# Kernel tuning notes

Measured on AMD Instinct MI355X. Metric: run time of the kernel, lower is better.

The kernel has to match this reference:

```python
import jax, jax.numpy as jnp
import numpy as np

LANDMARKS = 80
POINT_LANDMARKS = tuple(range(468, 538))  # 70 hand-region indices
AVG_SET = [[0,40],[40,40],[80,60],[140,60],[200,60],[260,60],[320,50],[370,50],[420,60],[480,63]]
STAT_CAP = 168


def nan_mean(x, axis=0):
    m = jnp.isnan(x)
    num = jnp.where(m, 0.0, x).sum(axis)
    den = jnp.where(m, 0.0, 1.0).sum(axis)
    return num / den


def nan_std(x, axis=0):
    d = x - nan_mean(x, axis=axis)
    return jnp.sqrt(nan_mean(d * d, axis=axis))


def flatten_means_and_stds(x, reshape1):
    # x: [t, L, C] -> stats over frames -> [2L, C] -> (1, reshape1*2)
    out = jnp.concatenate([nan_mean(x, 0), nan_std(x, 0)], axis=0)
    if out.shape[0] > STAT_CAP:
        out = out[:STAT_CAP, :]
    out = out.reshape(1, reshape1 * 2)
    return jnp.where(jnp.isfinite(out), out, jnp.zeros_like(out))


def setup_inputs() -> dict:
    key = jax.random.key(0)
    T, N, C = 32768, 543, 3
    x_in = jax.random.normal(key, (T, N, C), dtype=jnp.float32)
    return {
        "x_in": x_in,
        "num_frames": 16384,
        "segments": 4,
        "input_shape": (16384, 240),
    }


def reference(x_in, num_frames, segments, input_shape):
    # 1) cluster means + point gather -> x: [T, LANDMARKS, 3]
    parts = [jnp.mean(x_in[:, s:s + l, :], axis=1, keepdims=True) for s, l in AVG_SET]
    parts.append(x_in[:, jnp.array(POINT_LANDMARKS), :])
    x = jnp.concatenate(parts, axis=1)

    # 2) symmetric padding loop (axis 1), gated on T % segments as in the original
    xp = x
    rem = x.shape[0] % segments  # shapes are static -> Python int
    for i in range(segments):
        p0 = 1 if (rem > 0 and i % 2 != 0) else 0
        p1 = 1 if (rem > 0 and i % 2 == 0) else 0
        if p0 or p1:
            xp = jnp.pad(xp, ((0, 0), (p0, p1), (0, 0)), mode='symmetric')

    # 3) per-segment nan mean/std stats
    segs = np.array_split(np.arange(xp.shape[0]), segments)
    feats = [flatten_means_and_stds(xp[idx[0]:idx[-1] + 1], input_shape[1]) for idx in segs]
    feats.append(flatten_means_and_stds(x, input_shape[1]))

    # 4) bilinear resize (align_corners=False semantics, no antialias)
    xi = jnp.transpose(x, (2, 0, 1))[None]            # [1, 3, T, L]
    xi = jax.image.resize(xi, (1, 3, num_frames, LANDMARKS), method='bilinear', antialias=False)
    xi = jnp.transpose(xi[0], (1, 2, 0))              # [num_frames, L, 3]
    xi = xi.reshape(1, input_shape[0] * input_shape[1])
    xi = jnp.where(jnp.isnan(xi), jnp.zeros_like(xi), xi)
    feats.append(xi)

    return jnp.concatenate(feats, axis=1)
```

## Files before the change

### kernel.cpp

```cpp
#include <hip/hip_runtime.h>
#include <math.h>

#define T_FRAMES   32768
#define N_LM       543
#define FRAME      1629
#define FPB        16
#define NBLOCKS    (T_FRAMES / FPB)
#define TILES      4
#define TILE_F4    1629
#define OUT_B_OFF  2400
#define ACC_FLOATS 1920

__constant__ int   c_astart[10] = {0, 40, 80, 140, 200, 260, 320, 370, 420, 480};
__constant__ int   c_alen[10]   = {40, 40, 60, 60, 60, 60, 50, 50, 60, 63};

__global__ void zero_acc_kernel(float* __restrict__ acc) {
    int i = blockIdx.x * 256 + threadIdx.x;
    if (i < ACC_FLOATS) acc[i] = 0.0f;
}

__global__ __launch_bounds__(256, 6) void featgen_main(
    const float* __restrict__ xin, float* __restrict__ out, float* __restrict__ acc)
{
    __shared__ float rows[4 * FRAME];

    const int t = threadIdx.x;
    const int b = blockIdx.x;
    const float* src = xin + (size_t)b * (FPB * FRAME);

    const int g8 = t >> 3;
    const int j8 = t & 7;
    int a_s = 0, a_n = 0, a_c = 0;
    float a_inv = 0.0f;
    if (g8 < 30) {
        int l = g8 / 3; a_c = g8 - 3 * l;
        a_s = c_astart[l]; a_n = c_alen[l];
        a_inv = 1.0f / (float)a_n;
    }

    float ssum = 0.0f, ssq = 0.0f;
    float lsum = 0.0f, lsq = 0.0f;

    float4 pre[7];

    {
        const float4* s4 = (const float4*)src;
        #pragma unroll
        for (int i = 0; i < 7; ++i) {
            int idx = t + i * 256;
            if (idx < TILE_F4) pre[i] = s4[idx];
        }
        float4* d4 = (float4*)rows;
        #pragma unroll
        for (int i = 0; i < 7; ++i) {
            int idx = t + i * 256;
            if (idx < TILE_F4) d4[idx] = pre[i];
        }
    }
    __syncthreads();

    for (int grp = 0; grp < TILES; ++grp) {
        if (grp < TILES - 1) {
            const float4* s4 = (const float4*)(src + (size_t)(grp + 1) * (4 * FRAME));
            #pragma unroll
            for (int i = 0; i < 7; ++i) {
                int idx = t + i * 256;
                if (idx < TILE_F4) pre[i] = s4[idx];
            }
        }

        const size_t row0 = (size_t)b * (FPB / 2) + (size_t)grp * 2;

        if (g8 < 30) {
            float v[4];
            #pragma unroll
            for (int f = 0; f < 4; ++f) {
                const float* row = rows + f * FRAME;
                float s = 0.0f;
                for (int j = j8; j < a_n; j += 8) s += row[(a_s + j) * 3 + a_c];
                s += __shfl_xor(s, 1, 8);
                s += __shfl_xor(s, 2, 8);
                s += __shfl_xor(s, 4, 8);
                v[f] = s * a_inv;
            }
            if (j8 == 0) {
                out[OUT_B_OFF + row0 * 240 + g8]       = 0.5f * (v[0] + v[1]);
                out[OUT_B_OFF + (row0 + 1) * 240 + g8] = 0.5f * (v[2] + v[3]);
                lsum += v[0] + v[1] + v[2] + v[3];
                lsq  += v[0]*v[0] + v[1]*v[1] + v[2]*v[2] + v[3]*v[3];
            }
        }

        if (t >= 30 && t < 240) {
            float v0 = rows[0 * FRAME + t + 1374];
            float v1 = rows[1 * FRAME + t + 1374];
            float v2 = rows[2 * FRAME + t + 1374];
            float v3 = rows[3 * FRAME + t + 1374];
            out[OUT_B_OFF + row0 * 240 + t]       = 0.5f * (v0 + v1);
            out[OUT_B_OFF + (row0 + 1) * 240 + t] = 0.5f * (v2 + v3);
            ssum += v0 + v1 + v2 + v3;
            ssq  += v0*v0 + v1*v1 + v2*v2 + v3*v3;
        }

        __syncthreads();

        if (grp < TILES - 1) {
            float4* d4 = (float4*)rows;
            #pragma unroll
            for (int i = 0; i < 7; ++i) {
                int idx = t + i * 256;
                if (idx < TILE_F4) d4[idx] = pre[i];
            }
            __syncthreads();
        }
    }

    const int seg = b >> 9;
    if (g8 < 30 && j8 == 0) {
        atomicAdd(&acc[seg * 480 + g8],       lsum);
        atomicAdd(&acc[seg * 480 + 240 + g8], lsq);
    }
    if (t >= 30 && t < 240) {
        atomicAdd(&acc[seg * 480 + t],       ssum);
        atomicAdd(&acc[seg * 480 + 240 + t], ssq);
    }
}

__global__ __launch_bounds__(256) void finalize_stats(
    const float* __restrict__ acc, float* __restrict__ out)
{
    const int f = blockIdx.x;
    const int t = threadIdx.x;
    if (t >= 240) return;
    float s, q, n;
    if (f < 4) {
        s = acc[f * 480 + t];
        q = acc[f * 480 + 240 + t];
        n = 8192.0f;
    } else {
        s = acc[t]       + acc[480 + t]  + acc[960 + t]  + acc[1440 + t];
        q = acc[240 + t] + acc[720 + t]  + acc[1200 + t] + acc[1680 + t];
        n = 32768.0f;
    }
    float mean = s / n;
    float var  = q / n - mean * mean;
    var = var < 0.0f ? 0.0f : var;
    out[f * 480 + t]       = mean;
    out[f * 480 + 240 + t] = sqrtf(var);
}

extern "C" void kernel_launch(void* const* d_in, const int* in_sizes, int n_in,
                              void* d_out, int out_size, void* d_ws, size_t ws_size,
                              hipStream_t stream) {
    (void)in_sizes; (void)n_in; (void)out_size; (void)ws_size;
    const float* xin = (const float*)d_in[0];
    float* out = (float*)d_out;
    float* acc = (float*)d_ws;

    zero_acc_kernel<<<8, 256, 0, stream>>>(acc);
    featgen_main<<<NBLOCKS, 256, 0, stream>>>(xin, out, acc);
    finalize_stats<<<5, 256, 0, stream>>>(acc, out);
}
```

Measured before the change: 375.4 us.

## Stage frame tiles with async global_load_lds double buffering and bigger blocks

Replaces the register-staged prefetch (global load into registers, then LDS store) with direct global-to-LDS loads into a double-buffered shared tile, so each iteration issues the next tile's load and needs only one barrier. Frames per block double from 16 to 32, which halves the block count and adjusts the segment index. The launch-bounds occupancy hint is removed, and LDS per block grows to about 53 KB, which may reduce resident blocks per CU. Correctness depends on the async LDS load being complete at the barrier without an explicit vmcnt wait.

Result: faster. 311.1 us (-17.1%).

```diff
diff --git a/kernel.cpp b/kernel.cpp
--- a/kernel.cpp
+++ b/kernel.cpp
@@ -1,31 +1,57 @@
 #include <hip/hip_runtime.h>
 #include <math.h>
+#include <stdint.h>
 
 #define T_FRAMES   32768
 #define N_LM       543
 #define FRAME      1629
-#define FPB        16
+#define FPB        32
 #define NBLOCKS    (T_FRAMES / FPB)
-#define TILES      4
-#define TILE_F4    1629
+#define TILES      8
+#define TILE_BYTES 26064
+#define CHUNKS     26
+#define BUF_FLOATS 6660
 #define OUT_B_OFF  2400
 #define ACC_FLOATS 1920
 
 __constant__ int   c_astart[10] = {0, 40, 80, 140, 200, 260, 320, 370, 420, 480};
 __constant__ int   c_alen[10]   = {40, 40, 60, 60, 60, 60, 50, 50, 60, 63};
 
+typedef const __attribute__((address_space(1))) uint32_t* gas_ptr;
+typedef __attribute__((address_space(3)))       uint32_t* las_ptr;
+
 __global__ void zero_acc_kernel(float* __restrict__ acc) {
     int i = blockIdx.x * 256 + threadIdx.x;
     if (i < ACC_FLOATS) acc[i] = 0.0f;
 }
 
-__global__ __launch_bounds__(256, 6) void featgen_main(
+__device__ __forceinline__ void stage_tile(const float* __restrict__ gsrc,
+                                           float* lbase, int w, int lane)
+{
+    #pragma unroll
+    for (int i = 0; i < 7; ++i) {
+        int c = w + 4 * i;
+        if (c < CHUNKS) {
+            int off = c * 1024 + lane * 16;
+            if (off < TILE_BYTES) {
+                __builtin_amdgcn_global_load_lds(
+                    (gas_ptr)((const uint8_t*)gsrc + off),
+                    (las_ptr)((uint8_t*)lbase + c * 1024),
+                    16, 0, 0);
+            }
+        }
+    }
+}
+
+__global__ __launch_bounds__(256) void featgen_main(
     const float* __restrict__ xin, float* __restrict__ out, float* __restrict__ acc)
 {
-    __shared__ float rows[4 * FRAME];
+    __shared__ __align__(16) float buf[2][BUF_FLOATS];
 
-    const int t = threadIdx.x;
-    const int b = blockIdx.x;
+    const int t    = threadIdx.x;
+    const int b    = blockIdx.x;
+    const int w    = t >> 6;
+    const int lane = t & 63;
     const float* src = xin + (size_t)b * (FPB * FRAME);
 
     const int g8 = t >> 3;
@@ -41,33 +67,14 @@
     float ssum = 0.0f, ssq = 0.0f;
     float lsum = 0.0f, lsq = 0.0f;
 
-    float4 pre[7];
-
-    {
-        const float4* s4 = (const float4*)src;
-        #pragma unroll
-        for (int i = 0; i < 7; ++i) {
-            int idx = t + i * 256;
-            if (idx < TILE_F4) pre[i] = s4[idx];
-        }
-        float4* d4 = (float4*)rows;
-        #pragma unroll
-        for (int i = 0; i < 7; ++i) {
-            int idx = t + i * 256;
-            if (idx < TILE_F4) d4[idx] = pre[i];
-        }
-    }
+    stage_tile(src, buf[0], w, lane);
     __syncthreads();
 
     for (int grp = 0; grp < TILES; ++grp) {
-        if (grp < TILES - 1) {
-            const float4* s4 = (const float4*)(src + (size_t)(grp + 1) * (4 * FRAME));
-            #pragma unroll
-            for (int i = 0; i < 7; ++i) {
-                int idx = t + i * 256;
-                if (idx < TILE_F4) pre[i] = s4[idx];
-            }
-        }
+        const float* rows = buf[grp & 1];
+
+        if (grp < TILES - 1)
+            stage_tile(src + (size_t)(grp + 1) * (4 * FRAME), buf[(grp + 1) & 1], w, lane);
 
         const size_t row0 = (size_t)b * (FPB / 2) + (size_t)grp * 2;
 
@@ -103,19 +110,9 @@
         }
 
         __syncthreads();
-
-        if (grp < TILES - 1) {
-            float4* d4 = (float4*)rows;
-            #pragma unroll
-            for (int i = 0; i < 7; ++i) {
-                int idx = t + i * 256;
-                if (idx < TILE_F4) d4[idx] = pre[i];
-            }
-            __syncthreads();
-        }
     }
 
-    const int seg = b >> 9;
+    const int seg = b >> 8;
     if (g8 < 30 && j8 == 0) {
         atomicAdd(&acc[seg * 480 + g8],       lsum);
         atomicAdd(&acc[seg * 480 + 240 + g8], lsq);
```
